# Performance work log

Measured on AMD Instinct MI355X. Metric: run time of the kernel, lower is better.

The kernel has to match this reference:

```python
import jax, jax.numpy as jnp
import numpy as np

B, N, C = 4, 3136, 64
IMG_H = IMG_W = 56
HEADS = 1
TOPK = 8
HID = 4 * C  # mlp_ratio=4.0


def _ln(x, g, b, eps=1e-5):
    m = x.mean(-1, keepdims=True)
    v = ((x - m) ** 2).mean(-1, keepdims=True)
    return (x - m) * jax.lax.rsqrt(v + eps) * g + b


def _conv(x, w, b, pad, groups):
    y = jax.lax.conv_general_dilated(
        x, w, (1, 1), [(pad, pad), (pad, pad)],
        dimension_numbers=('NCHW', 'OIHW', 'NCHW'), feature_group_count=groups)
    return y + b[None, :, None, None]


def setup_inputs() -> dict:
    key = jax.random.key(0)
    ks = jax.random.split(key, 10)
    def rn(k, shp, scale=0.02):
        return jax.random.normal(k, shp, jnp.float32) * scale
    return {
        'x': jax.random.normal(ks[0], (B, N, C), jnp.float32),
        'norm1_g': jnp.ones((C,), jnp.float32), 'norm1_b': jnp.zeros((C,), jnp.float32),
        'wq': rn(ks[1], (C, C)), 'bq': jnp.zeros((C,), jnp.float32),
        'wkv': rn(ks[2], (C, 2 * C)), 'bkv': jnp.zeros((2 * C,), jnp.float32),
        'wproj': rn(ks[3], (C, C)), 'bproj': jnp.zeros((C,), jnp.float32),
        'local_w': rn(ks[4], (C, C // HEADS, 3, 3), 0.05), 'local_b': jnp.zeros((C,), jnp.float32),
        'norm2_g': jnp.ones((C,), jnp.float32), 'norm2_b': jnp.zeros((C,), jnp.float32),
        'w3': rn(ks[5], (HID, 1, 3, 3), 0.05), 'b3': jnp.zeros((HID,), jnp.float32),
        'w5': rn(ks[6], (HID, 1, 5, 5), 0.05), 'b5': jnp.zeros((HID,), jnp.float32),
        'w1': rn(ks[7], (C, 2 * HID, 1, 1), 0.05), 'b1': jnp.zeros((C,), jnp.float32),
        'H': IMG_H, 'W': IMG_W,
    }


def reference(x, norm1_g, norm1_b, wq, bq, wkv, bkv, wproj, bproj,
              local_w, local_b, norm2_g, norm2_b, w3, b3, w5, b5, w1, b1, H, W):
    Bb, Nn, Cc = x.shape
    d = Cc // HEADS
    scale = d ** -0.5
    # --- DynamicSparseAttention (global branch) ---
    xn = _ln(x, norm1_g, norm1_b)
    q = (xn @ wq + bq).reshape(Bb, Nn, HEADS, d).transpose(0, 2, 1, 3)       # bhnd
    kv = (xn @ wkv + bkv).reshape(Bb, Nn, 2, HEADS, d)
    k = kv[:, :, 0].transpose(0, 2, 1, 3)
    v = kv[:, :, 1].transpose(0, 2, 1, 3)
    attn = jnp.einsum('bhnd,bhmd->bhnm', q, k) * scale                        # [B,h,N,N]
    kth = jax.lax.top_k(attn, TOPK)[0][..., -1:]                              # k-th largest per row
    mask = (attn >= kth).astype(attn.dtype)                                   # top-k scatter mask
    p = jax.nn.softmax(attn * mask, axis=-1)                                  # zeros kept (as in torch ref)
    g = jnp.einsum('bhnm,bhmd->bhnd', p, v).transpose(0, 2, 1, 3).reshape(Bb, Nn, Cc)
    g = g @ wproj + bproj
    # --- local conv attention branch ---
    x_img = x.transpose(0, 2, 1).reshape(Bb, Cc, H, W)
    loc = _conv(x_img, local_w, local_b, 1, HEADS).reshape(Bb, Cc, Nn).transpose(0, 2, 1)
    # --- residual 1 (note: norm1 params reused, as in source) ---
    x = x + _ln(g + loc, norm1_g, norm1_b)
    # --- MSFN ---
    xn2 = _ln(x, norm2_g, norm2_b).transpose(0, 2, 1).reshape(Bb, Cc, H, W)
    x3 = _conv(xn2, w3, b3, 1, Cc)   # depthwise 3x3, channel mult 4
    x5 = _conv(xn2, w5, b5, 2, Cc)   # depthwise 5x5, channel mult 4
    m = _conv(jnp.concatenate([x3, x5], axis=1), w1, b1, 0, 1)
    return x + m.reshape(Bb, Cc, Nn).transpose(0, 2, 1)
```

## Files before the change

### kernel.cpp

```cpp
#include <hip/hip_runtime.h>
#include <math.h>

#define Bv 4
#define Nv 3136
#define Cv 64
#define Hh 56
#define Ww 56
#define HIDv 256
#define TOPKv 8
#define TSP 520
#define LCP 584
#define XNP 72
#define KSPL 16
#define KPS 196

constexpr float SCALE = 0.125f;
constexpr float EPS = 1e-5f;
constexpr float SBIAS = 128.0f;

typedef short bf16x8 __attribute__((ext_vector_type(8)));
typedef float f32x4 __attribute__((ext_vector_type(4)));

#define CSWAP(a, b) { unsigned int _hi = max(a, b); unsigned int _lo = min(a, b); a = _hi; b = _lo; }
#define BITONIC8(T) \
  CSWAP(T[0], T[4]); CSWAP(T[1], T[5]); CSWAP(T[2], T[6]); CSWAP(T[3], T[7]); \
  CSWAP(T[0], T[2]); CSWAP(T[1], T[3]); CSWAP(T[4], T[6]); CSWAP(T[5], T[7]); \
  CSWAP(T[0], T[1]); CSWAP(T[2], T[3]); CSWAP(T[4], T[5]); CSWAP(T[6], T[7]);

__device__ __forceinline__ unsigned short f2bf(float f) {
  unsigned int u = __float_as_uint(f);
  u = (u + 0x7FFFu + ((u >> 16) & 1u)) >> 16;
  return (unsigned short)u;
}
__device__ __forceinline__ float bf2f(unsigned short u) {
  return __uint_as_float(((unsigned int)u) << 16);
}
__device__ __forceinline__ unsigned int pack2(float a, float b) {
  return (unsigned int)f2bf(a) | ((unsigned int)f2bf(b) << 16);
}

__device__ __forceinline__ unsigned int packB(float sb, int j) {
  return (__float_as_uint(sb) & 0xFFFFF000u) | (unsigned int)j;
}

__global__ void k_transpose(const float* __restrict__ w1, const float* __restrict__ lw,
                            const float* __restrict__ w3, const float* __restrict__ w5,
                            const float* __restrict__ wq, const float* __restrict__ wkv,
                            const float* __restrict__ bq, const float* __restrict__ bkv,
                            const float* __restrict__ wproj,
                            unsigned short* __restrict__ w1bf, unsigned short* __restrict__ lwb,
                            float* __restrict__ w3t, float* __restrict__ w5t,
                            unsigned short* __restrict__ wqkvt, float* __restrict__ qkvb,
                            unsigned short* __restrict__ wprojt, float* __restrict__ sumv) {
  int p = blockIdx.x * 256 + threadIdx.x;
  if (p < 256) sumv[p] = 0.0f;
  if (p < 64 * 512) w1bf[p] = f2bf(w1[p]);
  if (p < 64 * 576) {
    int co = p / 576, k = p % 576;
    int tap = k >> 6, ci = k & 63;
    lwb[p] = f2bf(lw[co * 576 + ci * 9 + tap]);
  }
  if (p < 36 * 64) {
    int cin = p & 63, tm = p >> 6;
    int tap = tm >> 2, m = tm & 3;
    w3t[p] = w3[(cin * 4 + m) * 9 + tap];
  }
  if (p < 100 * 64) {
    int cin = p & 63, tm = p >> 6;
    int tap = tm >> 2, m = tm & 3;
    w5t[p] = w5[(cin * 4 + m) * 25 + tap];
  }
  if (p < 192 * 64) {
    int o = p >> 6, i = p & 63;
    float v = (o < 64) ? wq[i * 64 + o] : wkv[i * 128 + (o - 64)];
    wqkvt[p] = f2bf(v);
  }
  if (p < 192) qkvb[p] = (p < 64) ? bq[p] : bkv[p - 64];
  if (p < 64 * 64) {
    int o = p >> 6, i = p & 63;
    wprojt[p] = f2bf(wproj[i * 64 + o]);
  }
}

__global__ __launch_bounds__(256) void k_ln_qkv(
    const float* __restrict__ x, const float* __restrict__ g1, const float* __restrict__ b1,
    const unsigned short* __restrict__ wqkvt, const float* __restrict__ qkvb,
    unsigned short* __restrict__ q16, unsigned short* __restrict__ k16,
    float* __restrict__ vo, float* __restrict__ sumv) {
  __shared__ __align__(16) unsigned short xnS[16 * XNP];
  int bid = blockIdx.x;
  int b = bid / 196, tile = bid % 196;
  size_t tok0 = (size_t)b * Nv + tile * 16;
  int t = threadIdx.x;
  int w = t >> 6, l = t & 63;
  int tokL = t >> 4;
  int ch0 = (t & 15) * 4;
  size_t tok = tok0 + tokL;
  float v[4];
  *(float4*)v = *(const float4*)&x[tok * 64 + ch0];
  float s = v[0] + v[1] + v[2] + v[3];
  float s2 = v[0] * v[0] + v[1] * v[1] + v[2] * v[2] + v[3] * v[3];
#pragma unroll
  for (int off = 1; off <= 8; off <<= 1) {
    s += __shfl_xor(s, off, 64);
    s2 += __shfl_xor(s2, off, 64);
  }
  float m = s * (1.f / 64.f);
  float rs = rsqrtf(s2 * (1.f / 64.f) - m * m + EPS);
  {
    unsigned int pk[2];
    float a0_ = (v[0] - m) * rs * g1[ch0] + b1[ch0];
    float a1_ = (v[1] - m) * rs * g1[ch0 + 1] + b1[ch0 + 1];
    float a2_ = (v[2] - m) * rs * g1[ch0 + 2] + b1[ch0 + 2];
    float a3_ = (v[3] - m) * rs * g1[ch0 + 3] + b1[ch0 + 3];
    pk[0] = pack2(a0_, a1_);
    pk[1] = pack2(a2_, a3_);
    *(uint2*)&xnS[tokL * XNP + ch0] = *(uint2*)pk;
  }
  __syncthreads();
  int n = l & 15, q = l >> 4;
  const bf16x8 a0 = *(const bf16x8*)&xnS[n * XNP + q * 8];
  const bf16x8 a1 = *(const bf16x8*)&xnS[n * XNP + 32 + q * 8];
  {
    const unsigned short* wr = &wqkvt[(size_t)(w * 16 + n) * 64];
    bf16x8 b0 = *(const bf16x8*)&wr[q * 8];
    bf16x8 b1_ = *(const bf16x8*)&wr[32 + q * 8];
    f32x4 acc = {0.f, 0.f, 0.f, 0.f};
    acc = __builtin_amdgcn_mfma_f32_16x16x32_bf16(a0, b0, acc, 0, 0, 0);
    acc = __builtin_amdgcn_mfma_f32_16x16x32_bf16(a1, b1_, acc, 0, 0, 0);
    float bias = qkvb[w * 16 + n];
#pragma unroll
    for (int r = 0; r < 4; ++r)
      q16[(tok0 + q * 4 + r) * 64 + w * 16 + n] = f2bf(acc[r] + bias);
  }
  {
    const unsigned short* wr = &wqkvt[(size_t)((w + 4) * 16 + n) * 64];
    bf16x8 b0 = *(const bf16x8*)&wr[q * 8];
    bf16x8 b1_ = *(const bf16x8*)&wr[32 + q * 8];
    f32x4 acc = {0.f, 0.f, 0.f, 0.f};
    acc = __builtin_amdgcn_mfma_f32_16x16x32_bf16(a0, b0, acc, 0, 0, 0);
    acc = __builtin_amdgcn_mfma_f32_16x16x32_bf16(a1, b1_, acc, 0, 0, 0);
    float bias = qkvb[64 + w * 16 + n];
#pragma unroll
    for (int r = 0; r < 4; ++r)
      k16[(tok0 + q * 4 + r) * 64 + w * 16 + n] = f2bf(acc[r] + bias);
  }
  {
    const unsigned short* wr = &wqkvt[(size_t)((w + 8) * 16 + n) * 64];
    bf16x8 b0 = *(const bf16x8*)&wr[q * 8];
    bf16x8 b1_ = *(const bf16x8*)&wr[32 + q * 8];
    f32x4 acc = {0.f, 0.f, 0.f, 0.f};
    acc = __builtin_amdgcn_mfma_f32_16x16x32_bf16(a0, b0, acc, 0, 0, 0);
    acc = __builtin_amdgcn_mfma_f32_16x16x32_bf16(a1, b1_, acc, 0, 0, 0);
    float bias = qkvb[128 + w * 16 + n];
    float vp = acc[0] + acc[1] + acc[2] + acc[3] + 4.0f * bias;
#pragma unroll
    for (int r = 0; r < 4; ++r)
      vo[(tok0 + q * 4 + r) * 64 + w * 16 + n] = acc[r] + bias;
    vp += __shfl_xor(vp, 16, 64);
    vp += __shfl_xor(vp, 32, 64);
    if (q == 0) atomicAdd(&sumv[b * 64 + w * 16 + n], vp);
  }
}

#define PAIRMERGE(T, accA, accB, jb) { \
    unsigned int _p0 = packB(accA[0], (jb) + 0); \
    unsigned int _p1 = packB(accA[1], (jb) + 1); \
    unsigned int _p2 = packB(accA[2], (jb) + 2); \
    unsigned int _p3 = packB(accA[3], (jb) + 3); \
    unsigned int _q0 = packB(accB[0], (jb) + 16); \
    unsigned int _q1 = packB(accB[1], (jb) + 17); \
    unsigned int _q2 = packB(accB[2], (jb) + 18); \
    unsigned int _q3 = packB(accB[3], (jb) + 19); \
    CSWAP(_p0, _p1); CSWAP(_p2, _p3); CSWAP(_p0, _p2); CSWAP(_p1, _p3); CSWAP(_p1, _p2); \
    CSWAP(_q0, _q1); CSWAP(_q2, _q3); CSWAP(_q0, _q2); CSWAP(_q1, _q3); CSWAP(_q1, _q2); \
    unsigned int _u8[8] = {_p0, _p1, _p2, _p3, _q3, _q2, _q1, _q0}; \
    BITONIC8(_u8); \
    T[0] = max(T[0], _u8[7]); \
    T[1] = max(T[1], _u8[6]); \
    T[2] = max(T[2], _u8[5]); \
    T[3] = max(T[3], _u8[4]); \
    T[4] = max(T[4], _u8[3]); \
    T[5] = max(T[5], _u8[2]); \
    T[6] = max(T[6], _u8[1]); \
    T[7] = max(T[7], _u8[0]); \
    BITONIC8(T); }

__global__ __launch_bounds__(128, 3) void k_attn_topk(
    const unsigned short* __restrict__ q16, const unsigned short* __restrict__ k16,
    unsigned int* __restrict__ top8out) {
  int bid = blockIdx.x;
  int w = threadIdx.x >> 6;
  int lane = threadIdx.x & 63;
  int split = ((bid & 7) << 1) | w;
  int lin = bid >> 3;
  int b = lin / 49, tg = lin % 49;
  int qbase = b * Nv + tg * 64;
  size_t bN = (size_t)b * Nv;
  int qcol = lane & 15, quad = lane >> 4;
  int quad4 = quad * 4;

  bf16x8 qf0a[4], qf1a[4];
#pragma unroll
  for (int tt = 0; tt < 4; ++tt) {
    qf0a[tt] = *(const bf16x8*)&q16[((size_t)(qbase + tt * 16 + qcol)) * 64 + quad * 8];
    qf1a[tt] = *(const bf16x8*)&q16[((size_t)(qbase + tt * 16 + qcol)) * 64 + 32 + quad * 8];
  }

  unsigned int t8[4][8];
#pragma unroll
  for (int tt = 0; tt < 4; ++tt)
#pragma unroll
    for (int u = 0; u < 8; ++u) t8[tt][u] = 0u;

  int kbase = split * KPS;
  int m = lane & 15;
  const char* kbp = (const char*)(k16 + bN * 64);
  unsigned int offA = (unsigned int)((kbase + m) * 128 + quad * 16);
  int jbA = kbase + quad4;

  bf16x8 ka0 = *(const bf16x8*)(kbp + offA);
  bf16x8 ka1 = *(const bf16x8*)(kbp + offA + 64);
  bf16x8 kb0 = *(const bf16x8*)(kbp + offA + 2048);
  bf16x8 kb1 = *(const bf16x8*)(kbp + offA + 2112);
  offA += 4096;

#pragma unroll 1
  for (int it = 0; it < 5; ++it) {
    bf16x8 ca0 = ka0, ca1 = ka1, cb0 = kb0, cb1 = kb1;
    ka0 = *(const bf16x8*)(kbp + offA);
    ka1 = *(const bf16x8*)(kbp + offA + 64);
    kb0 = *(const bf16x8*)(kbp + offA + 2048);
    kb1 = *(const bf16x8*)(kbp + offA + 2112);
    offA += 4096;

#pragma unroll
    for (int tt = 0; tt < 4; ++tt) {
      f32x4 accA = {SBIAS, SBIAS, SBIAS, SBIAS};
      accA = __builtin_amdgcn_mfma_f32_16x16x32_bf16(ca0, qf0a[tt], accA, 0, 0, 0);
      accA = __builtin_amdgcn_mfma_f32_16x16x32_bf16(ca1, qf1a[tt], accA, 0, 0, 0);
      f32x4 accB = {SBIAS, SBIAS, SBIAS, SBIAS};
      accB = __builtin_amdgcn_mfma_f32_16x16x32_bf16(cb0, qf0a[tt], accB, 0, 0, 0);
      accB = __builtin_amdgcn_mfma_f32_16x16x32_bf16(cb1, qf1a[tt], accB, 0, 0, 0);
      PAIRMERGE(t8[tt], accA, accB, jbA);
    }
    jbA += 32;
  }

  {
    bf16x8 ca0 = ka0, ca1 = ka1, cb0 = kb0, cb1 = kb1;
    ka0 = *(const bf16x8*)(kbp + offA);
    ka1 = *(const bf16x8*)(kbp + offA + 64);

#pragma unroll
    for (int tt = 0; tt < 4; ++tt) {
      f32x4 accA = {SBIAS, SBIAS, SBIAS, SBIAS};
      accA = __builtin_amdgcn_mfma_f32_16x16x32_bf16(ca0, qf0a[tt], accA, 0, 0, 0);
      accA = __builtin_amdgcn_mfma_f32_16x16x32_bf16(ca1, qf1a[tt], accA, 0, 0, 0);
      f32x4 accB = {SBIAS, SBIAS, SBIAS, SBIAS};
      accB = __builtin_amdgcn_mfma_f32_16x16x32_bf16(cb0, qf0a[tt], accB, 0, 0, 0);
      accB = __builtin_amdgcn_mfma_f32_16x16x32_bf16(cb1, qf1a[tt], accB, 0, 0, 0);
      PAIRMERGE(t8[tt], accA, accB, jbA);
    }
    jbA += 32;
  }

  {
    int klim = kbase + KPS;
#pragma unroll
    for (int tt = 0; tt < 4; ++tt) {
      f32x4 accA = {SBIAS, SBIAS, SBIAS, SBIAS};
      accA = __builtin_amdgcn_mfma_f32_16x16x32_bf16(ka0, qf0a[tt], accA, 0, 0, 0);
      accA = __builtin_amdgcn_mfma_f32_16x16x32_bf16(ka1, qf1a[tt], accA, 0, 0, 0);
      unsigned int p0 = (jbA + 0 < klim) ? packB(accA[0], jbA + 0) : 0u;
      unsigned int p1 = (jbA + 1 < klim) ? packB(accA[1], jbA + 1) : 0u;
      unsigned int p2 = (jbA + 2 < klim) ? packB(accA[2], jbA + 2) : 0u;
      unsigned int p3 = (jbA + 3 < klim) ? packB(accA[3], jbA + 3) : 0u;
      CSWAP(p0, p1); CSWAP(p2, p3); CSWAP(p0, p2); CSWAP(p1, p3); CSWAP(p1, p2);
      t8[tt][4] = max(t8[tt][4], p3);
      t8[tt][5] = max(t8[tt][5], p2);
      t8[tt][6] = max(t8[tt][6], p1);
      t8[tt][7] = max(t8[tt][7], p0);
      BITONIC8(t8[tt]);
    }
  }

#pragma unroll
  for (int tt = 0; tt < 4; ++tt) {
#pragma unroll
    for (int step = 16; step <= 32; step <<= 1) {
      unsigned int o[8];
#pragma unroll
      for (int i = 0; i < 8; ++i) o[i] = (unsigned int)__shfl_xor((int)t8[tt][i], step, 64);
      unsigned int nw[8];
#pragma unroll
      for (int i = 0; i < 8; ++i) nw[i] = max(t8[tt][i], o[7 - i]);
#pragma unroll
      for (int i = 0; i < 8; ++i) t8[tt][i] = nw[i];
      BITONIC8(t8[tt]);
    }
    if (quad == 0) {
      size_t obase = ((size_t)(bN + tg * 64 + tt * 16 + qcol)) * 128 + split * 8;
      *(uint4*)&top8out[obase] = make_uint4(t8[tt][0], t8[tt][1], t8[tt][2], t8[tt][3]);
      *(uint4*)&top8out[obase + 4] = make_uint4(t8[tt][4], t8[tt][5], t8[tt][6], t8[tt][7]);
    }
  }
}

__global__ __launch_bounds__(256) void k_attn_proj(
    const unsigned int* __restrict__ top8, const float* __restrict__ vg,
    const float* __restrict__ sumv, const float* __restrict__ x,
    const unsigned short* __restrict__ lwb, const float* __restrict__ lb,
    const unsigned short* __restrict__ wprojt, const float* __restrict__ bproj,
    const float* __restrict__ g1, const float* __restrict__ b1,
    const float* __restrict__ g2, const float* __restrict__ b2,
    float* __restrict__ x2, unsigned short* __restrict__ xn2b) {
  __shared__ float kwS[16][8];
  __shared__ int kidxS[16][8];
  __shared__ float invZS[16];
  __shared__ __align__(16) unsigned short imS[16 * LCP];
  __shared__ __align__(16) unsigned short gS[16 * XNP];
  __shared__ float yS[16 * 66];
  int bid = blockIdx.x;
  int b = bid / 196, rem = bid % 196;
  int th = rem / 7, tw = rem % 7;
  int h0 = th * 2, w0 = tw * 8;
  size_t bN = (size_t)b * Nv;
  int t = threadIdx.x;

  if (t < 64) {
    int tk = t >> 2, la = t & 3;
    int gtok = (h0 + (tk >> 3)) * Ww + w0 + (tk & 7);
    size_t base = (bN + gtok) * 128 + la * 32;
    unsigned int A[8];
#pragma unroll
    for (int i = 0; i < 8; ++i) A[i] = top8[base + i];
#pragma unroll
    for (int h = 1; h < 4; ++h) {
      unsigned int Bb[8];
#pragma unroll
      for (int i = 0; i < 8; ++i) Bb[i] = top8[base + h * 8 + i];
#pragma unroll
      for (int i = 0; i < 8; ++i) A[i] = max(A[i], Bb[7 - i]);
      BITONIC8(A);
    }
#pragma unroll
    for (int step = 1; step <= 2; step <<= 1) {
      unsigned int o[8];
#pragma unroll
      for (int i = 0; i < 8; ++i) o[i] = (unsigned int)__shfl_xor((int)A[i], step, 64);
#pragma unroll
      for (int i = 0; i < 8; ++i) A[i] = max(A[i], o[7 - i]);
      BITONIC8(A);
    }
    if (la == 0) {
      float Z = (float)(Nv - TOPKv);
#pragma unroll
      for (int u = 0; u < 8; ++u) {
        float sb = __uint_as_float(A[u] & 0xFFFFF000u);
        float s = (sb - SBIAS) * SCALE;
        float e = __expf(s);
        kwS[tk][u] = e - 1.0f;
        kidxS[tk][u] = (int)(A[u] & 0xFFFu);
        Z += e;
      }
      invZS[tk] = 1.0f / Z;
    }
  } else {
    for (int p = t - 64; p < 1152; p += 192) {
      int sub = p & 7, s = p >> 3;
      int tok = s / 9, tap = s % 9;
      int tr = tok >> 3, tc = tok & 7;
      int dh = tap / 3, dw = tap % 3;
      int gh = h0 + tr - 1 + dh, gw = w0 + tc - 1 + dw;
      uint4 uu = {0u, 0u, 0u, 0u};
      if (gh >= 0 && gh < Hh && gw >= 0 && gw < Ww) {
        const float* xp = &x[(bN + gh * Ww + gw) * 64 + sub * 8];
        float4 va = *(const float4*)xp;
        float4 vb = *(const float4*)(xp + 4);
        uu.x = pack2(va.x, va.y);
        uu.y = pack2(va.z, va.w);
        uu.z = pack2(vb.x, vb.y);
        uu.w = pack2(vb.z, vb.w);
      }
      *(uint4*)&imS[tok * LCP + tap * 64 + sub * 8] = uu;
    }
  }
  __syncthreads();

  int w = t >> 6, l = t & 63;
  int n = l & 15, q = l >> 4;

  int c = t & 63, rg = t >> 6;
  float vgv[4][8];
#pragma unroll
  for (int rr = 0; rr < 4; ++rr) {
    int tokL = rg * 4 + rr;
#pragma unroll
    for (int u = 0; u < 8; ++u)
      vgv[rr][u] = vg[(bN + kidxS[tokL][u]) * 64 + c];
  }

  f32x4 lacc = {0.f, 0.f, 0.f, 0.f};
  {
    const unsigned short* lwrow = &lwb[(size_t)(w * 16 + n) * 576];
#pragma unroll 6
    for (int kk = 0; kk < 18; ++kk) {
      bf16x8 af = *(const bf16x8*)&imS[n * LCP + kk * 32 + q * 8];
      bf16x8 bfr = *(const bf16x8*)&lwrow[kk * 32 + q * 8];
      lacc = __builtin_amdgcn_mfma_f32_16x16x32_bf16(af, bfr, lacc, 0, 0, 0);
    }
  }
  float lbias = lb[w * 16 + n];

  {
    float sv = sumv[b * 64 + c];
#pragma unroll
    for (int rr = 0; rr < 4; ++rr) {
      int tokL = rg * 4 + rr;
      float acc = sv;
#pragma unroll
      for (int u = 0; u < 8; ++u)
        acc += kwS[tokL][u] * vgv[rr][u];
      gS[tokL * XNP + c] = f2bf(acc * invZS[tokL]);
    }
  }
  __syncthreads();

  {
    const bf16x8 a0 = *(const bf16x8*)&gS[n * XNP + q * 8];
    const bf16x8 a1 = *(const bf16x8*)&gS[n * XNP + 32 + q * 8];
    const unsigned short* wr = &wprojt[(size_t)(w * 16 + n) * 64];
    bf16x8 b0 = *(const bf16x8*)&wr[q * 8];
    bf16x8 b1_ = *(const bf16x8*)&wr[32 + q * 8];
    f32x4 acc = {0.f, 0.f, 0.f, 0.f};
    acc = __builtin_amdgcn_mfma_f32_16x16x32_bf16(a0, b0, acc, 0, 0, 0);
    acc = __builtin_amdgcn_mfma_f32_16x16x32_bf16(a1, b1_, acc, 0, 0, 0);
    float bias = bproj[w * 16 + n];
#pragma unroll
    for (int r = 0; r < 4; ++r)
      yS[(q * 4 + r) * 66 + w * 16 + n] = acc[r] + bias + lacc[r] + lbias;
  }
  __syncthreads();

  int tokL = t >> 4;
  int ch0 = (t & 15) * 4;
  size_t tok = bN + (size_t)(h0 + (tokL >> 3)) * Ww + w0 + (tokL & 7);
  float y[4];
#pragma unroll
  for (int i = 0; i < 4; ++i) y[i] = yS[tokL * 66 + ch0 + i];
  float s = y[0] + y[1] + y[2] + y[3];
  float s2 = y[0] * y[0] + y[1] * y[1] + y[2] * y[2] + y[3] * y[3];
#pragma unroll
  for (int off = 1; off <= 8; off <<= 1) {
    s += __shfl_xor(s, off, 64);
    s2 += __shfl_xor(s2, off, 64);
  }
  float m1 = s * (1.f / 64.f);
  float rs1 = rsqrtf(s2 * (1.f / 64.f) - m1 * m1 + EPS);
  float xv[4];
  *(float4*)xv = *(const float4*)&x[tok * 64 + ch0];
  float x2v[4];
  float t_s = 0.f, t_s2 = 0.f;
#pragma unroll
  for (int i = 0; i < 4; ++i) {
    float t1 = (y[i] - m1) * rs1 * g1[ch0 + i] + b1[ch0 + i];
    x2v[i] = xv[i] + t1;
    t_s += x2v[i];
    t_s2 += x2v[i] * x2v[i];
  }
#pragma unroll
  for (int off = 1; off <= 8; off <<= 1) {
    t_s += __shfl_xor(t_s, off, 64);
    t_s2 += __shfl_xor(t_s2, off, 64);
  }
  float m2 = t_s * (1.f / 64.f);
  float rs2 = rsqrtf(t_s2 * (1.f / 64.f) - m2 * m2 + EPS);
  *(float4*)&x2[tok * 64 + ch0] = *(float4*)x2v;
  unsigned int pk[2];
  {
    float a0_ = (x2v[0] - m2) * rs2 * g2[ch0] + b2[ch0];
    float a1_ = (x2v[1] - m2) * rs2 * g2[ch0 + 1] + b2[ch0 + 1];
    float a2_ = (x2v[2] - m2) * rs2 * g2[ch0 + 2] + b2[ch0 + 2];
    float a3_ = (x2v[3] - m2) * rs2 * g2[ch0 + 3] + b2[ch0 + 3];
    pk[0] = pack2(a0_, a1_);
    pk[1] = pack2(a2_, a3_);
  }
  *(uint2*)&xn2b[tok * 64 + ch0] = *(uint2*)pk;
}

__global__ __launch_bounds__(256) void k_msfn(
    const unsigned short* __restrict__ xn2b, const float* __restrict__ x2,
    const float* __restrict__ w3t, const float* __restrict__ b3,
    const float* __restrict__ w5t, const float* __restrict__ b5,
    const unsigned short* __restrict__ w1bf, const float* __restrict__ b1,
    float* __restrict__ out) {
  __shared__ __align__(16) unsigned short xtS[6 * 12 * 64];
  __shared__ __align__(16) unsigned short tsS[16 * TSP];

  int bid = blockIdx.x;
  int b = bid / 196;
  int rem = bid % 196;
  int th = rem / 7, tw = rem % 7;
  int h0 = th * 2, w0 = tw * 8;
  size_t bN = (size_t)b * Nv;
  int t = threadIdx.x;

  unsigned int* xtU = (unsigned int*)xtS;
  for (int p = t; p < 6 * 12 * 32; p += 256) {
    int cp = p & 31, rc = p >> 5;
    int r = rc / 12, cc = rc % 12;
    int gh = h0 - 2 + r, gw = w0 - 2 + cc;
    unsigned int v = 0;
    if (gh >= 0 && gh < Hh && gw >= 0 && gw < Ww)
      v = *(const unsigned int*)&xn2b[(bN + gh * Ww + gw) * 64 + cp * 2];
    xtU[rc * 32 + cp] = v;
  }
  __syncthreads();

  int cin = t & 63, tg = t >> 6;
  int tr = tg >> 1, tc0 = (tg & 1) * 4;
  float win[5][8];
#pragma unroll
  for (int r = 0; r < 5; ++r)
#pragma unroll
    for (int c = 0; c < 8; ++c)
      win[r][c] = bf2f(xtS[((tr + r) * 12 + tc0 + c) * 64 + cin]);

  unsigned int* tsU = (unsigned int*)tsS;
#pragma unroll 1
  for (int m2 = 0; m2 < 4; m2 += 2) {
    float a3[2][9], a5[2][25], bb3[2], bb5[2];
#pragma unroll
    for (int mm = 0; mm < 2; ++mm) {
      int m = m2 + mm;
#pragma unroll
      for (int tap = 0; tap < 9; ++tap) a3[mm][tap] = w3t[(tap * 4 + m) * 64 + cin];
#pragma unroll
      for (int tap = 0; tap < 25; ++tap) a5[mm][tap] = w5t[(tap * 4 + m) * 64 + cin];
      bb3[mm] = b3[cin * 4 + m];
      bb5[mm] = b5[cin * 4 + m];
    }
#pragma unroll
    for (int tk = 0; tk < 4; ++tk) {
      int tok = tg * 4 + tk;
      unsigned int p3 = 0, p5 = 0;
#pragma unroll
      for (int mm = 0; mm < 2; ++mm) {
        float acc3 = bb3[mm];
#pragma unroll
        for (int kh = 0; kh < 3; ++kh)
#pragma unroll
          for (int kw2 = 0; kw2 < 3; ++kw2)
            acc3 += win[1 + kh][tk + 1 + kw2] * a3[mm][kh * 3 + kw2];
        float acc5 = bb5[mm];
#pragma unroll
        for (int kh = 0; kh < 5; ++kh)
#pragma unroll
          for (int kw2 = 0; kw2 < 5; ++kw2)
            acc5 += win[kh][tk + kw2] * a5[mm][kh * 5 + kw2];
        p3 |= (unsigned int)f2bf(acc3) << (16 * mm);
        p5 |= (unsigned int)f2bf(acc5) << (16 * mm);
      }
      tsU[(tok * TSP + cin * 4 + m2) >> 1] = p3;
      tsU[(tok * TSP + 256 + cin * 4 + m2) >> 1] = p5;
    }
  }
  __syncthreads();

  int wv = tg, lane = t & 63;
  int n16 = lane & 15, quad = lane >> 4;
  const unsigned short* wrow = &w1bf[(size_t)(wv * 16 + n16) * 512];
  f32x4 acc = {0.f, 0.f, 0.f, 0.f};
#pragma unroll 4
  for (int kk = 0; kk < 16; ++kk) {
    bf16x8 af = *(const bf16x8*)&tsS[n16 * TSP + kk * 32 + quad * 8];
    bf16x8 bfr = *(const bf16x8*)&wrow[kk * 32 + quad * 8];
    acc = __builtin_amdgcn_mfma_f32_16x16x32_bf16(af, bfr, acc, 0, 0, 0);
  }
  float bias = b1[wv * 16 + n16];
#pragma unroll
  for (int r = 0; r < 4; ++r) {
    int tok = quad * 4 + r;
    int trr = tok >> 3, tcc = tok & 7;
    size_t idx = (bN + (size_t)(h0 + trr) * Ww + w0 + tcc) * 64 + wv * 16 + n16;
    out[idx] = x2[idx] + acc[r] + bias;
  }
}

extern "C" void kernel_launch(void* const* d_in, const int* in_sizes, int n_in,
                              void* d_out, int out_size, void* d_ws, size_t ws_size,
                              hipStream_t stream) {
  const float* x = (const float*)d_in[0];
  const float* n1g = (const float*)d_in[1];
  const float* n1b = (const float*)d_in[2];
  const float* wq = (const float*)d_in[3];
  const float* bq = (const float*)d_in[4];
  const float* wkv = (const float*)d_in[5];
  const float* bkv = (const float*)d_in[6];
  const float* wproj = (const float*)d_in[7];
  const float* bproj = (const float*)d_in[8];
  const float* lw = (const float*)d_in[9];
  const float* lb = (const float*)d_in[10];
  const float* n2g = (const float*)d_in[11];
  const float* n2b = (const float*)d_in[12];
  const float* w3 = (const float*)d_in[13];
  const float* b3 = (const float*)d_in[14];
  const float* w5 = (const float*)d_in[15];
  const float* b5 = (const float*)d_in[16];
  const float* w1 = (const float*)d_in[17];
  const float* b1 = (const float*)d_in[18];
  float* out = (float*)d_out;

  float* ws = (float*)d_ws;
  const size_t TOK = (size_t)Bv * Nv * Cv;
  float* vb = ws;
  float* sumv = vb + TOK;
  float* x2 = sumv + 256;
  float* w3t = x2 + TOK;
  float* w5t = w3t + 2304;
  float* qkvb = w5t + 6400;
  unsigned short* q16 = (unsigned short*)(qkvb + 192);
  unsigned short* k16 = q16 + TOK;
  unsigned short* xn2b = k16 + TOK;
  unsigned short* w1bf = xn2b + TOK;
  unsigned short* lwb = w1bf + 64 * 512;
  unsigned short* wqkvt = lwb + 64 * 576;
  unsigned short* wprojt = wqkvt + 192 * 64;
  unsigned int* top8ws = (unsigned int*)(wprojt + 64 * 64 + 64);

  k_transpose<<<144, 256, 0, stream>>>(w1, lw, w3, w5, wq, wkv, bq, bkv, wproj,
                                       w1bf, lwb, w3t, w5t, wqkvt, qkvb, wprojt, sumv);
  k_ln_qkv<<<Bv * 196, 256, 0, stream>>>(x, n1g, n1b, wqkvt, qkvb, q16, k16, vb, sumv);
  k_attn_topk<<<Bv * 49 * 8, 128, 0, stream>>>(q16, k16, top8ws);
  k_attn_proj<<<Bv * 196, 256, 0, stream>>>(top8ws, vb, sumv, x, lwb, lb, wprojt, bproj,
                                            n1g, n1b, n2g, n2b, x2, xn2b);
  k_msfn<<<Bv * 196, 256, 0, stream>>>(xn2b, x2, w3t, b3, w5t, b5, w1bf, b1, out);
}
```

Before: 171.1 us.

## Stage K split chunk in swizzled LDS shared by two query-tile waves

Reorganises the top-k attention kernel so each block copies one K split (208 rows) into LDS with an XOR swizzle, and its two waves then score two different 64-query tiles against that shared chunk. Previously each wave streamed its own K split from global memory with register double-buffering. The goal is to halve global/L2 K traffic per query tile and avoid bank conflicts on the LDS reads. In exchange it adds a block-wide barrier and a serial staging phase with no overlap against MFMA work, and the grid grows slightly so a few waves exit idle.

Measured after the change: 171.0 us. No clear change (-0.1%).

```diff
diff --git a/kernel.cpp b/kernel.cpp
--- a/kernel.cpp
+++ b/kernel.cpp
@@ -189,16 +189,32 @@
 __global__ __launch_bounds__(128, 3) void k_attn_topk(
     const unsigned short* __restrict__ q16, const unsigned short* __restrict__ k16,
     unsigned int* __restrict__ top8out) {
+  __shared__ __align__(16) unsigned short kS[13312];
   int bid = blockIdx.x;
-  int w = threadIdx.x >> 6;
-  int lane = threadIdx.x & 63;
-  int split = ((bid & 7) << 1) | w;
-  int lin = bid >> 3;
-  int b = lin / 49, tg = lin % 49;
+  int t = threadIdx.x;
+  int w = t >> 6;
+  int lane = t & 63;
+  int tgp = bid % 25;
+  int bs = bid / 25;
+  int b = bs >> 4, split = bs & 15;
+  int tg = tgp * 2 + w;
+  size_t bN = (size_t)b * Nv;
+  int kbase = split * KPS;
+
+  {
+    const char* src = (const char*)(k16 + bN * 64) + kbase * 128 + t * 16;
+    char* dst = (char*)kS + (t >> 3) * 128 + (((t & 7) ^ ((t >> 3) & 7)) << 4);
+#pragma unroll
+    for (int r = 0; r < 13; ++r)
+      *(uint4*)(dst + r * 2048) = *(const uint4*)(src + r * 2048);
+  }
+  __syncthreads();
+  if (tg >= 49) return;
+
   int qbase = b * Nv + tg * 64;
-  size_t bN = (size_t)b * Nv;
   int qcol = lane & 15, quad = lane >> 4;
   int quad4 = quad * 4;
+  int m = lane & 15;
 
   bf16x8 qf0a[4], qf1a[4];
 #pragma unroll
@@ -213,26 +229,17 @@
 #pragma unroll
     for (int u = 0; u < 8; ++u) t8[tt][u] = 0u;
 
-  int kbase = split * KPS;
-  int m = lane & 15;
-  const char* kbp = (const char*)(k16 + bN * 64);
-  unsigned int offA = (unsigned int)((kbase + m) * 128 + quad * 16);
   int jbA = kbase + quad4;
-
-  bf16x8 ka0 = *(const bf16x8*)(kbp + offA);
-  bf16x8 ka1 = *(const bf16x8*)(kbp + offA + 64);
-  bf16x8 kb0 = *(const bf16x8*)(kbp + offA + 2048);
-  bf16x8 kb1 = *(const bf16x8*)(kbp + offA + 2112);
-  offA += 4096;
+  int swz = m & 7;
+  const char* pa = (const char*)kS + m * 128 + ((quad ^ swz) << 4);
+  const char* pb = (const char*)kS + m * 128 + (((quad + 4) ^ swz) << 4);
 
 #pragma unroll 1
-  for (int it = 0; it < 5; ++it) {
-    bf16x8 ca0 = ka0, ca1 = ka1, cb0 = kb0, cb1 = kb1;
-    ka0 = *(const bf16x8*)(kbp + offA);
-    ka1 = *(const bf16x8*)(kbp + offA + 64);
-    kb0 = *(const bf16x8*)(kbp + offA + 2048);
-    kb1 = *(const bf16x8*)(kbp + offA + 2112);
-    offA += 4096;
+  for (int it = 0; it < 6; ++it) {
+    bf16x8 ca0 = *(const bf16x8*)(pa + it * 4096);
+    bf16x8 ca1 = *(const bf16x8*)(pb + it * 4096);
+    bf16x8 cb0 = *(const bf16x8*)(pa + it * 4096 + 2048);
+    bf16x8 cb1 = *(const bf16x8*)(pb + it * 4096 + 2048);
 
 #pragma unroll
     for (int tt = 0; tt < 4; ++tt) {
@@ -248,24 +255,8 @@
   }
 
   {
-    bf16x8 ca0 = ka0, ca1 = ka1, cb0 = kb0, cb1 = kb1;
-    ka0 = *(const bf16x8*)(kbp + offA);
-    ka1 = *(const bf16x8*)(kbp + offA + 64);
-
-#pragma unroll
-    for (int tt = 0; tt < 4; ++tt) {
-      f32x4 accA = {SBIAS, SBIAS, SBIAS, SBIAS};
-      accA = __builtin_amdgcn_mfma_f32_16x16x32_bf16(ca0, qf0a[tt], accA, 0, 0, 0);
-      accA = __builtin_amdgcn_mfma_f32_16x16x32_bf16(ca1, qf1a[tt], accA, 0, 0, 0);
-      f32x4 accB = {SBIAS, SBIAS, SBIAS, SBIAS};
-      accB = __builtin_amdgcn_mfma_f32_16x16x32_bf16(cb0, qf0a[tt], accB, 0, 0, 0);
-      accB = __builtin_amdgcn_mfma_f32_16x16x32_bf16(cb1, qf1a[tt], accB, 0, 0, 0);
-      PAIRMERGE(t8[tt], accA, accB, jbA);
-    }
-    jbA += 32;
-  }
-
-  {
+    bf16x8 ka0 = *(const bf16x8*)(pa + 12 * 2048);
+    bf16x8 ka1 = *(const bf16x8*)(pb + 12 * 2048);
     int klim = kbase + KPS;
 #pragma unroll
     for (int tt = 0; tt < 4; ++tt) {
@@ -632,7 +623,7 @@
   k_transpose<<<144, 256, 0, stream>>>(w1, lw, w3, w5, wq, wkv, bq, bkv, wproj,
                                        w1bf, lwb, w3t, w5t, wqkvt, qkvb, wprojt, sumv);
   k_ln_qkv<<<Bv * 196, 256, 0, stream>>>(x, n1g, n1b, wqkvt, qkvb, q16, k16, vb, sumv);
-  k_attn_topk<<<Bv * 49 * 8, 128, 0, stream>>>(q16, k16, top8ws);
+  k_attn_topk<<<Bv * 16 * 25, 128, 0, stream>>>(q16, k16, top8ws);
   k_attn_proj<<<Bv * 196, 256, 0, stream>>>(top8ws, vb, sumv, x, lwb, lb, wprojt, bproj,
                                             n1g, n1b, n2g, n2b, x2, xn2b);
   k_msfn<<<Bv * 196, 256, 0, stream>>>(xn2b, x2, w3t, b3, w5t, b5, w1bf, b1, out);
```
